# Kernel optimization log

Hardware: AMD Instinct MI355X
Metric: run time of the kernel (lower is better)

## Reference

```python
import jax, jax.numpy as jnp
import numpy as np

GAMMA = 0.1
BATCH, NUM_SV, DIM = 8192, 8192, 256


def setup_inputs() -> dict:
    key = jax.random.key(0)
    k1, k2, k3 = jax.random.split(key, 3)
    x = jax.random.normal(k1, (BATCH, DIM), dtype=jnp.float32)
    support_vectors = jax.random.normal(k2, (NUM_SV, DIM), dtype=jnp.float32)
    dual_coefficients = jax.random.normal(k3, (NUM_SV,), dtype=jnp.float32)
    return {"x": x, "support_vectors": support_vectors, "dual_coefficients": dual_coefficients}


def reference(x, support_vectors, dual_coefficients):
    # Squared Euclidean distance via the GEMM expansion (same math as
    # sum((x[:,None,:]-sv[None,:,:])**2, -1) without the (B, S, D) intermediate).
    x_sq = jnp.sum(x * x, axis=-1, keepdims=True)            # (B, 1)
    sv_sq = jnp.sum(support_vectors * support_vectors, -1)   # (S,)
    cross = jnp.einsum('bd,sd->bs', x, support_vectors)      # (B, S)
    sq_dist = jnp.maximum(x_sq + sv_sq[None, :] - 2.0 * cross, 0.0)
    kernel_matrix = jnp.exp(-GAMMA * sq_dist)                # (B, S)
    return jnp.einsum('bs,s->b', kernel_matrix, dual_coefficients)
```

## Files before the change

kernel.cpp:

```cpp
#include <hip/hip_runtime.h>

#define BATCH 8192
#define NUM_SV 8192
#define DIM 256
#define GAMMA 0.1f
#define LOG2E 1.4426950408889634f
#define ALPHA 0.53715827f

#define SCHUNK 8
#define NST 4
#define NKC 8
#define NITER (NST * NKC)
#define TILE_F16 8192

typedef _Float16 f16;
typedef __attribute__((ext_vector_type(8))) _Float16 f16x8;
typedef __attribute__((ext_vector_type(16))) float f32x16;

__device__ __forceinline__ void gload_lds16(const f16* g, f16* l) {
  __builtin_amdgcn_global_load_lds((const __attribute__((address_space(1))) void*)g,
                                   (__attribute__((address_space(3))) void*)l, 16, 0, 0);
}

__global__ __launch_bounds__(256)
void svm_prep(const float* __restrict__ x, const float* __restrict__ sv,
              const float* __restrict__ dual,
              f16* __restrict__ x16, f16* __restrict__ sv16,
              float* __restrict__ xg, float* __restrict__ dcp) {
  const int id = blockIdx.x * 256 + threadIdx.x;
  const bool isx = id < (BATCH * DIM / 8);
  const int lid = isx ? id : id - (BATCH * DIM / 8);
  const int row = lid >> 5;
  const int k0  = (lid & 31) << 3;

  const float* src = (isx ? x : sv) + (size_t)row * DIM + k0;
  float4 u = *(const float4*)(src);
  float4 v = *(const float4*)(src + 4);

  float sq = u.x*u.x + u.y*u.y + u.z*u.z + u.w*u.w
           + v.x*v.x + v.y*v.y + v.z*v.z + v.w*v.w;
  #pragma unroll
  for (int m = 1; m <= 16; m <<= 1) sq += __shfl_xor(sq, m, 32);
  if ((lid & 31) == 0) {
    float g = -(GAMMA * LOG2E) * sq;
    if (isx) xg[row] = g;
    else     dcp[row] = dual[row] * __builtin_amdgcn_exp2f(g);
  }

  f16x8 h;
  h[0] = (f16)(ALPHA * u.x); h[1] = (f16)(ALPHA * u.y);
  h[2] = (f16)(ALPHA * u.z); h[3] = (f16)(ALPHA * u.w);
  h[4] = (f16)(ALPHA * v.x); h[5] = (f16)(ALPHA * v.y);
  h[6] = (f16)(ALPHA * v.z); h[7] = (f16)(ALPHA * v.w);

  const int bt = row >> 8;
  const int r  = row & 255;
  const int kc = k0 >> 5;
  const int c  = (k0 >> 3) & 3;
  f16* dst = (isx ? x16 : sv16) + (size_t)(bt * NKC + kc) * TILE_F16 + (c * 256 + r) * 8;
  *(f16x8*)dst = h;
}

__global__ __launch_bounds__(512, 2)
void svm_main(const f16* __restrict__ x16, const f16* __restrict__ sv16,
              const float* __restrict__ dcp, float* __restrict__ partial) {
  __shared__ f16 lds[3][2 * TILE_F16];
  __shared__ float dcpl[NST * 256];

  const int tid = threadIdx.x;
  const int w   = tid >> 6;
  const int l   = tid & 63;
  const int lr  = l & 31;
  const int lh  = l >> 5;
  const int wb  = w >> 1;
  const int wn  = w & 1;
  const int sch = blockIdx.x;
  const int bt  = blockIdx.y;
  const int stile0 = sch * NST;

  {
    float2 dv2 = *(const float2*)&dcp[stile0 * 256 + tid * 2];
    *(float2*)&dcpl[tid * 2] = dv2;
  }
  __syncthreads();

  auto stage = [&](f16* dst, int stile, int kc) {
    const f16* xb = x16  + (size_t)(bt * NKC + kc) * TILE_F16;
    const f16* sb = sv16 + (size_t)(stile * NKC + kc) * TILE_F16;
    #pragma unroll
    for (int j = 0; j < 4; ++j) {
      const int r = w * 4 + j;
      const f16* src = (r < 16) ? (xb + r * 512 + l * 8)
                                : (sb + (r - 16) * 512 + l * 8);
      gload_lds16(src, dst + r * 512);
    }
  };

  float ctr[2][16];
  #pragma unroll
  for (int m = 0; m < 2; ++m)
    #pragma unroll
    for (int r = 0; r < 16; ++r) ctr[m][r] = 0.f;

  stage(&lds[0][0], stile0, 0);
  stage(&lds[1][0], stile0, 1);
  int ib = 0;

  #pragma unroll 1
  for (int st = 0; st < NST; ++st) {
    f32x16 acc[2][4];
    #pragma unroll
    for (int m = 0; m < 2; ++m)
      #pragma unroll
      for (int n = 0; n < 4; ++n)
        #pragma unroll
        for (int r = 0; r < 16; ++r) acc[m][n][r] = 0.f;

    #pragma unroll 1
    for (int kc = 0; kc < NKC; ++kc) {
      __builtin_amdgcn_sched_barrier(0);
      if (st == NST - 1 && kc == NKC - 1)
        asm volatile("s_waitcnt vmcnt(0)" ::: "memory");
      else
        asm volatile("s_waitcnt vmcnt(4)" ::: "memory");
      __builtin_amdgcn_s_barrier();
      __builtin_amdgcn_sched_barrier(0);

      const int t2 = st * NKC + kc + 2;
      int ib2 = ib + 2; if (ib2 >= 3) ib2 -= 3;
      if (t2 < NITER)
        stage(&lds[ib2][0], stile0 + (t2 >> 3), t2 & 7);

      const f16* buf = &lds[ib][0];
      #pragma unroll
      for (int ks = 0; ks < 2; ++ks) {
        const int ko = (ks * 2 + lh) * 256;
        f16x8 a0 = *(const f16x8*)&buf[(ko + wb * 64 +  0 + lr) * 8];
        f16x8 a1 = *(const f16x8*)&buf[(ko + wb * 64 + 32 + lr) * 8];
        f16x8 b0 = *(const f16x8*)&buf[TILE_F16 + (ko + wn * 128 +  0 + lr) * 8];
        f16x8 b1 = *(const f16x8*)&buf[TILE_F16 + (ko + wn * 128 + 32 + lr) * 8];
        f16x8 b2 = *(const f16x8*)&buf[TILE_F16 + (ko + wn * 128 + 64 + lr) * 8];
        f16x8 b3 = *(const f16x8*)&buf[TILE_F16 + (ko + wn * 128 + 96 + lr) * 8];
        __builtin_amdgcn_s_setprio(1);
        acc[0][0] = __builtin_amdgcn_mfma_f32_32x32x16_f16(a0, b0, acc[0][0], 0, 0, 0);
        acc[0][1] = __builtin_amdgcn_mfma_f32_32x32x16_f16(a0, b1, acc[0][1], 0, 0, 0);
        acc[0][2] = __builtin_amdgcn_mfma_f32_32x32x16_f16(a0, b2, acc[0][2], 0, 0, 0);
        acc[0][3] = __builtin_amdgcn_mfma_f32_32x32x16_f16(a0, b3, acc[0][3], 0, 0, 0);
        acc[1][0] = __builtin_amdgcn_mfma_f32_32x32x16_f16(a1, b0, acc[1][0], 0, 0, 0);
        acc[1][1] = __builtin_amdgcn_mfma_f32_32x32x16_f16(a1, b1, acc[1][1], 0, 0, 0);
        acc[1][2] = __builtin_amdgcn_mfma_f32_32x32x16_f16(a1, b2, acc[1][2], 0, 0, 0);
        acc[1][3] = __builtin_amdgcn_mfma_f32_32x32x16_f16(a1, b3, acc[1][3], 0, 0, 0);
        __builtin_amdgcn_s_setprio(0);
      }
      ib = ib + 1; if (ib >= 3) ib -= 3;
    }

    #pragma unroll
    for (int n = 0; n < 4; ++n) {
      const float dv = dcpl[st * 256 + wn * 128 + n * 32 + lr];
      #pragma unroll
      for (int m = 0; m < 2; ++m)
        #pragma unroll
        for (int r = 0; r < 16; ++r)
          ctr[m][r] = fmaf(__builtin_amdgcn_exp2f(acc[m][n][r]), dv, ctr[m][r]);
    }
  }

  #pragma unroll
  for (int m = 0; m < 2; ++m)
    #pragma unroll
    for (int r = 0; r < 16; ++r) {
      float v = ctr[m][r];
      v += __shfl_xor(v, 1, 64);
      v += __shfl_xor(v, 2, 64);
      v += __shfl_xor(v, 4, 64);
      v += __shfl_xor(v, 8, 64);
      v += __shfl_xor(v, 16, 64);
      ctr[m][r] = v;
    }

  __syncthreads();
  float* red = (float*)&lds[0][0];
  if (lr == 0) {
    #pragma unroll
    for (int m = 0; m < 2; ++m)
      #pragma unroll
      for (int r = 0; r < 16; ++r) {
        const int rl = wb * 64 + m * 32 + (r & 3) + 8 * (r >> 2) + 4 * lh;
        red[wn * 256 + rl] = ctr[m][r];
      }
  }
  __syncthreads();
  if (tid < 256)
    partial[(size_t)sch * BATCH + bt * 256 + tid] = red[tid] + red[256 + tid];
}

__global__ __launch_bounds__(256)
void svm_reduce(const float* __restrict__ partial, const float* __restrict__ xg,
                float* __restrict__ out) {
  const int b = blockIdx.x * 256 + threadIdx.x;
  float s = 0.f;
  #pragma unroll
  for (int c = 0; c < SCHUNK; ++c) s += partial[(size_t)c * BATCH + b];
  out[b] = __builtin_amdgcn_exp2f(xg[b]) * s;
}

extern "C" void kernel_launch(void* const* d_in, const int* in_sizes, int n_in,
                              void* d_out, int out_size, void* d_ws, size_t ws_size,
                              hipStream_t stream) {
  const float* x    = (const float*)d_in[0];
  const float* sv   = (const float*)d_in[1];
  const float* dual = (const float*)d_in[2];
  float* out = (float*)d_out;

  f16*   x16     = (f16*)d_ws;
  f16*   sv16    = x16 + (size_t)BATCH * DIM;
  float* xg      = (float*)(sv16 + (size_t)NUM_SV * DIM);
  float* dcp     = xg + BATCH;
  float* partial = dcp + NUM_SV;

  svm_prep<<<(BATCH + NUM_SV) * DIM / 8 / 256, 256, 0, stream>>>(x, sv, dual, x16, sv16, xg, dcp);
  svm_main<<<dim3(SCHUNK, BATCH / 256), 512, 0, stream>>>(x16, sv16, dcp, partial);
  svm_reduce<<<BATCH / 256, 256, 0, stream>>>(partial, xg, out);
}
```

Before: 60.76 us.

## Switch to double-buffered 64-wide K tiles with plain block barriers

The main GEMM loop moves from a triple-buffered pipeline with 32-wide K chunks to a double-buffered pipeline with 64-wide K tiles. It drops the hand-tuned vmcnt waits, sched_barriers and setprio hints and uses __syncthreads. Each block-wide sync now covers twice as many MFMAs, which halves the number of barriers per block. The cost is a shorter prefetch distance (one tile ahead instead of two), a larger LDS footprint, and coarser, compiler-chosen waits on the global-to-LDS loads.

After: 55.03 us. 1.1x faster.

```diff
diff --git a/kernel.cpp b/kernel.cpp
--- a/kernel.cpp
+++ b/kernel.cpp
@@ -9,9 +9,10 @@
 
 #define SCHUNK 8
 #define NST 4
-#define NKC 8
-#define NITER (NST * NKC)
-#define TILE_F16 8192
+#define NKT 4
+#define NITER (NST * NKT)
+#define KC_F16 8192
+#define KT_F16 16384
 
 typedef _Float16 f16;
 typedef __attribute__((ext_vector_type(8))) _Float16 f16x8;
@@ -57,14 +58,14 @@
   const int r  = row & 255;
   const int kc = k0 >> 5;
   const int c  = (k0 >> 3) & 3;
-  f16* dst = (isx ? x16 : sv16) + (size_t)(bt * NKC + kc) * TILE_F16 + (c * 256 + r) * 8;
+  f16* dst = (isx ? x16 : sv16) + (size_t)(bt * 8 + kc) * KC_F16 + (c * 256 + r) * 8;
   *(f16x8*)dst = h;
 }
 
 __global__ __launch_bounds__(512, 2)
 void svm_main(const f16* __restrict__ x16, const f16* __restrict__ sv16,
               const float* __restrict__ dcp, float* __restrict__ partial) {
-  __shared__ f16 lds[3][2 * TILE_F16];
+  __shared__ f16 lds[2][2 * KT_F16];
   __shared__ float dcpl[NST * 256];
 
   const int tid = threadIdx.x;
@@ -82,17 +83,15 @@
     float2 dv2 = *(const float2*)&dcp[stile0 * 256 + tid * 2];
     *(float2*)&dcpl[tid * 2] = dv2;
   }
-  __syncthreads();
-
-  auto stage = [&](f16* dst, int stile, int kc) {
-    const f16* xb = x16  + (size_t)(bt * NKC + kc) * TILE_F16;
-    const f16* sb = sv16 + (size_t)(stile * NKC + kc) * TILE_F16;
-    #pragma unroll
-    for (int j = 0; j < 4; ++j) {
-      const int r = w * 4 + j;
-      const f16* src = (r < 16) ? (xb + r * 512 + l * 8)
-                                : (sb + (r - 16) * 512 + l * 8);
-      gload_lds16(src, dst + r * 512);
+
+  auto stage = [&](f16* dst, int stile, int kt) {
+    const f16* xA = x16  + (size_t)(bt * 8 + kt * 2) * KC_F16;
+    const f16* sB = sv16 + (size_t)(stile * 8 + kt * 2) * KC_F16;
+    #pragma unroll
+    for (int i = 0; i < 8; ++i) {
+      const int q = i * 512 + tid;
+      const f16* src = (i < 4) ? (xA + q * 8) : (sB + (q - 2048) * 8);
+      gload_lds16(src, dst + q * 8);
     }
   };
 
@@ -103,8 +102,6 @@
     for (int r = 0; r < 16; ++r) ctr[m][r] = 0.f;
 
   stage(&lds[0][0], stile0, 0);
-  stage(&lds[1][0], stile0, 1);
-  int ib = 0;
 
   #pragma unroll 1
   for (int st = 0; st < NST; ++st) {
@@ -117,42 +114,38 @@
         for (int r = 0; r < 16; ++r) acc[m][n][r] = 0.f;
 
     #pragma unroll 1
-    for (int kc = 0; kc < NKC; ++kc) {
-      __builtin_amdgcn_sched_barrier(0);
-      if (st == NST - 1 && kc == NKC - 1)
-        asm volatile("s_waitcnt vmcnt(0)" ::: "memory");
-      else
-        asm volatile("s_waitcnt vmcnt(4)" ::: "memory");
-      __builtin_amdgcn_s_barrier();
-      __builtin_amdgcn_sched_barrier(0);
-
-      const int t2 = st * NKC + kc + 2;
-      int ib2 = ib + 2; if (ib2 >= 3) ib2 -= 3;
-      if (t2 < NITER)
-        stage(&lds[ib2][0], stile0 + (t2 >> 3), t2 & 7);
-
-      const f16* buf = &lds[ib][0];
-      #pragma unroll
-      for (int ks = 0; ks < 2; ++ks) {
-        const int ko = (ks * 2 + lh) * 256;
-        f16x8 a0 = *(const f16x8*)&buf[(ko + wb * 64 +  0 + lr) * 8];
-        f16x8 a1 = *(const f16x8*)&buf[(ko + wb * 64 + 32 + lr) * 8];
-        f16x8 b0 = *(const f16x8*)&buf[TILE_F16 + (ko + wn * 128 +  0 + lr) * 8];
-        f16x8 b1 = *(const f16x8*)&buf[TILE_F16 + (ko + wn * 128 + 32 + lr) * 8];
-        f16x8 b2 = *(const f16x8*)&buf[TILE_F16 + (ko + wn * 128 + 64 + lr) * 8];
-        f16x8 b3 = *(const f16x8*)&buf[TILE_F16 + (ko + wn * 128 + 96 + lr) * 8];
-        __builtin_amdgcn_s_setprio(1);
-        acc[0][0] = __builtin_amdgcn_mfma_f32_32x32x16_f16(a0, b0, acc[0][0], 0, 0, 0);
-        acc[0][1] = __builtin_amdgcn_mfma_f32_32x32x16_f16(a0, b1, acc[0][1], 0, 0, 0);
-        acc[0][2] = __builtin_amdgcn_mfma_f32_32x32x16_f16(a0, b2, acc[0][2], 0, 0, 0);
-        acc[0][3] = __builtin_amdgcn_mfma_f32_32x32x16_f16(a0, b3, acc[0][3], 0, 0, 0);
-        acc[1][0] = __builtin_amdgcn_mfma_f32_32x32x16_f16(a1, b0, acc[1][0], 0, 0, 0);
-        acc[1][1] = __builtin_amdgcn_mfma_f32_32x32x16_f16(a1, b1, acc[1][1], 0, 0, 0);
-        acc[1][2] = __builtin_amdgcn_mfma_f32_32x32x16_f16(a1, b2, acc[1][2], 0, 0, 0);
-        acc[1][3] = __builtin_amdgcn_mfma_f32_32x32x16_f16(a1, b3, acc[1][3], 0, 0, 0);
-        __builtin_amdgcn_s_setprio(0);
+    for (int kt = 0; kt < NKT; ++kt) {
+      const int t = st * NKT + kt;
+      __syncthreads();
+
+      if (t + 1 < NITER) {
+        const int t1 = t + 1;
+        stage(&lds[t1 & 1][0], stile0 + (t1 >> 2), t1 & 3);
       }
-      ib = ib + 1; if (ib >= 3) ib -= 3;
+
+      const f16* bufA = &lds[t & 1][0];
+      const f16* bufB = bufA + KT_F16;
+      #pragma unroll
+      for (int ks2 = 0; ks2 < 2; ++ks2) {
+        #pragma unroll
+        for (int ks = 0; ks < 2; ++ks) {
+          const int ko = ks2 * KC_F16 / 8 + (ks * 2 + lh) * 256;
+          f16x8 a0 = *(const f16x8*)&bufA[(ko + wb * 64 +  0 + lr) * 8];
+          f16x8 a1 = *(const f16x8*)&bufA[(ko + wb * 64 + 32 + lr) * 8];
+          f16x8 b0 = *(const f16x8*)&bufB[(ko + wn * 128 +  0 + lr) * 8];
+          f16x8 b1 = *(const f16x8*)&bufB[(ko + wn * 128 + 32 + lr) * 8];
+          f16x8 b2 = *(const f16x8*)&bufB[(ko + wn * 128 + 64 + lr) * 8];
+          f16x8 b3 = *(const f16x8*)&bufB[(ko + wn * 128 + 96 + lr) * 8];
+          acc[0][0] = __builtin_amdgcn_mfma_f32_32x32x16_f16(a0, b0, acc[0][0], 0, 0, 0);
+          acc[0][1] = __builtin_amdgcn_mfma_f32_32x32x16_f16(a0, b1, acc[0][1], 0, 0, 0);
+          acc[0][2] = __builtin_amdgcn_mfma_f32_32x32x16_f16(a0, b2, acc[0][2], 0, 0, 0);
+          acc[0][3] = __builtin_amdgcn_mfma_f32_32x32x16_f16(a0, b3, acc[0][3], 0, 0, 0);
+          acc[1][0] = __builtin_amdgcn_mfma_f32_32x32x16_f16(a1, b0, acc[1][0], 0, 0, 0);
+          acc[1][1] = __builtin_amdgcn_mfma_f32_32x32x16_f16(a1, b1, acc[1][1], 0, 0, 0);
+          acc[1][2] = __builtin_amdgcn_mfma_f32_32x32x16_f16(a1, b2, acc[1][2], 0, 0, 0);
+          acc[1][3] = __builtin_amdgcn_mfma_f32_32x32x16_f16(a1, b3, acc[1][3], 0, 0, 0);
+        }
+      }
     }
 
     #pragma unroll
```
